# Performance work log

Measured on AMD Instinct MI355X. Metric: run time of the kernel, lower is better.

The kernel has to match this reference:

```python
import jax, jax.numpy as jnp
from jax import lax
import numpy as np

B, T, S = 64, 1024, 1024  # batch, seq_len, hidden size


def setup_inputs() -> dict:
    key = jax.random.key(0)
    ks = jax.random.split(key, 7)
    bound = 1.0 / np.sqrt(S)  # PyTorch GRU/Linear default init: U(-1/sqrt(H), 1/sqrt(H))
    u = lambda k, shape: jax.random.uniform(k, shape, jnp.float32, -bound, bound)
    return {
        "batch": jax.random.normal(ks[0], (B, T, S), jnp.float32),
        "W_ih": u(ks[1], (3 * S, S)),   # [r; z; n] input weights
        "W_hh": u(ks[2], (3 * S, S)),   # [r; z; n] hidden weights
        "b_ih": u(ks[3], (3 * S,)),
        "b_hh": u(ks[4], (3 * S,)),
        "W_out": u(ks[5], (1, S)),
        "b_out": u(ks[6], (1,)),
    }


def reference(batch, W_ih, W_hh, b_ih, b_hh, W_out, b_out):
    # Precompute input projections for all timesteps with one big GEMM: [B,T,3S]
    x_gates = jnp.einsum("bts,gs->btg", batch, W_ih) + b_ih

    def step(h, xg):
        # h: [B,S], xg: [B,3S]
        hg = h @ W_hh.T + b_hh                      # [B,3S]
        xr, xz, xn = jnp.split(xg, 3, axis=-1)
        hr, hz, hn = jnp.split(hg, 3, axis=-1)
        r = jax.nn.sigmoid(xr + hr)
        z = jax.nn.sigmoid(xz + hz)
        n = jnp.tanh(xn + r * hn)
        h_new = (1.0 - z) * n + z * h               # PyTorch GRU update
        return h_new, None

    h0 = jnp.zeros((batch.shape[0], S), batch.dtype)
    hT, _ = lax.scan(step, h0, jnp.swapaxes(x_gates, 0, 1))  # scan over time

    # last-timestep hidden -> linear -> sigmoid -> squeeze
    out = jax.nn.sigmoid(hT @ W_out.T + b_out)  # [B,1]
    return out.squeeze(-1)                      # [B]
```

## Files before the change

kernel.cpp:

```cpp
#include <hip/hip_runtime.h>
#include <math.h>


#define BB 64
#define TT 1024
#define SS 1024
#define GG (3 * SS)

__global__ void zero_kernel(float* __restrict__ p) {
  p[(size_t)blockIdx.x * 1024 + threadIdx.x] = 0.f;
}

__global__ __launch_bounds__(256) void xgates_kernel(
    const float* __restrict__ A, const float* __restrict__ W,
    const float* __restrict__ b_ih, const float* __restrict__ b_hh,
    float* __restrict__ C) {
  __shared__ float As[16][132];
  __shared__ float Bs[16][132];

  const int tid = threadIdx.x;
  const int n0 = blockIdx.x * 128;
  const int t0 = blockIdx.y * 2;
  const int tx = tid & 15;
  const int ty = tid >> 4;

  float acc[8][8];
#pragma unroll
  for (int i = 0; i < 8; ++i)
#pragma unroll
    for (int j = 0; j < 8; ++j) acc[i][j] = 0.f;

  for (int kt = 0; kt < SS / 16; ++kt) {
    const int k0 = kt * 16;
#pragma unroll
    for (int i = 0; i < 2; ++i) {
      const int idx = tid + i * 256;
      const int r = idx >> 2;
      const int kq = (idx & 3) * 4;
      float4 av = *(const float4*)&A[((size_t)(r & 63) * TT + t0 + (r >> 6)) * SS + k0 + kq];
      float4 bv = *(const float4*)&W[(size_t)(n0 + r) * SS + k0 + kq];
      As[kq + 0][r] = av.x; As[kq + 1][r] = av.y;
      As[kq + 2][r] = av.z; As[kq + 3][r] = av.w;
      Bs[kq + 0][r] = bv.x; Bs[kq + 1][r] = bv.y;
      Bs[kq + 2][r] = bv.z; Bs[kq + 3][r] = bv.w;
    }
    __syncthreads();
#pragma unroll
    for (int k = 0; k < 16; ++k) {
      float4 a0 = *(const float4*)&As[k][ty * 8];
      float4 a1 = *(const float4*)&As[k][ty * 8 + 4];
      float4 b0 = *(const float4*)&Bs[k][tx * 8];
      float4 b1 = *(const float4*)&Bs[k][tx * 8 + 4];
      float a[8] = {a0.x, a0.y, a0.z, a0.w, a1.x, a1.y, a1.z, a1.w};
      float b[8] = {b0.x, b0.y, b0.z, b0.w, b1.x, b1.y, b1.z, b1.w};
#pragma unroll
      for (int i = 0; i < 8; ++i)
#pragma unroll
        for (int j = 0; j < 8; ++j) acc[i][j] = fmaf(a[i], b[j], acc[i][j]);
    }
    __syncthreads();
  }

  float bias[8];
#pragma unroll
  for (int j = 0; j < 8; ++j) {
    const int n = n0 + tx * 8 + j;
    bias[j] = b_ih[n] + (n < 2 * SS ? b_hh[n] : 0.f);
  }
  const int tt = t0 + (ty >> 3);
  const int bbase = (ty & 7) * 8;
#pragma unroll
  for (int j = 0; j < 8; ++j) {
    const int n = n0 + tx * 8 + j;
    const int g = n >> 10;
    const int u = n & 1023;
    const size_t o = ((size_t)(tt * 3 + g) * SS + u) * 64 + bbase;
    *(float4*)&C[o] = make_float4(acc[0][j] + bias[j], acc[1][j] + bias[j],
                                  acc[2][j] + bias[j], acc[3][j] + bias[j]);
    *(float4*)&C[o + 4] = make_float4(acc[4][j] + bias[j], acc[5][j] + bias[j],
                                      acc[6][j] + bias[j], acc[7][j] + bias[j]);
  }
}

__global__ __launch_bounds__(1024) void gru_step_kernel(
    const float* __restrict__ hin, float* __restrict__ hout,
    const float* __restrict__ Whh, const float* __restrict__ xgT,
    const float* __restrict__ bhh, const int t) {
  __shared__ float part[16][64][13];
  __shared__ float sums[64][13];

  const int tid = threadIdx.x;
  const int lane = tid & 63;
  const int u0 = blockIdx.x * 4;
  const int wv = __builtin_amdgcn_readfirstlane(tid >> 6);
  const int k0 = wv * 64;

  const float* Wrow[12];
#pragma unroll
  for (int g = 0; g < 3; ++g)
#pragma unroll
    for (int r = 0; r < 4; ++r)
      Wrow[g * 4 + r] = Whh + (size_t)(g * SS + u0 + r) * SS + k0;

  float xr = 0.f, xz = 0.f, xn = 0.f, hold = 0.f, bhn = 0.f;
  if (tid < 256) {
    const int ur = tid >> 6;
    const size_t xb = ((size_t)(t * 3) * SS + u0 + ur) * 64 + (size_t)lane;
    xr = xgT[xb];
    xz = xgT[xb + (size_t)SS * 64];
    xn = xgT[xb + (size_t)2 * SS * 64];
    hold = hin[(u0 + ur) * 64 + lane];
    bhn = bhh[2 * SS + u0 + ur];
  }

  float acc[12];
#pragma unroll
  for (int i = 0; i < 12; ++i) acc[i] = 0.f;

  for (int kk = 0; kk < 64; kk += 8) {
    float hv[8];
#pragma unroll
    for (int e = 0; e < 8; ++e)
      hv[e] = hin[(size_t)(k0 + kk + e) * 64 + lane];
#pragma unroll
    for (int i = 0; i < 12; ++i) {
      const float* wp = Wrow[i] + kk;
      const float4 wa = *(const float4*)wp;
      const float4 wb = *(const float4*)(wp + 4);
      float a = acc[i];
      a = fmaf(hv[0], wa.x, a);
      a = fmaf(hv[1], wa.y, a);
      a = fmaf(hv[2], wa.z, a);
      a = fmaf(hv[3], wa.w, a);
      a = fmaf(hv[4], wb.x, a);
      a = fmaf(hv[5], wb.y, a);
      a = fmaf(hv[6], wb.z, a);
      a = fmaf(hv[7], wb.w, a);
      acc[i] = a;
    }
  }

  const int w = tid >> 6;
#pragma unroll
  for (int i = 0; i < 12; ++i) part[w][lane][i] = acc[i];
  __syncthreads();

  if (tid < 768) {
    const int sb = tid & 63, si = tid >> 6;
    float v = 0.f;
#pragma unroll
    for (int ww = 0; ww < 16; ++ww) v += part[ww][sb][si];
    sums[sb][si] = v;
  }
  __syncthreads();

  if (tid < 256) {
    const int ur = tid >> 6;
    const float ar = sums[lane][ur];
    const float az = sums[lane][4 + ur];
    const float an = sums[lane][8 + ur];
    const float rg = 1.f / (1.f + expf(-(xr + ar)));
    const float zg = 1.f / (1.f + expf(-(xz + az)));
    const float ng = tanhf(xn + rg * (an + bhn));
    hout[(u0 + ur) * 64 + lane] = (1.f - zg) * ng + zg * hold;
  }
}

__global__ __launch_bounds__(256) void out_kernel(
    const float* __restrict__ hT, const float* __restrict__ Wout,
    const float* __restrict__ bout, float* __restrict__ out) {
  const int b = blockIdx.x;
  const int tid = threadIdx.x;
  float s = 0.f;
#pragma unroll
  for (int i = 0; i < 4; ++i) {
    const int u = tid + i * 256;
    s = fmaf(hT[(size_t)u * 64 + b], Wout[u], s);
  }
#pragma unroll
  for (int off = 32; off; off >>= 1) s += __shfl_down(s, off);
  __shared__ float red[4];
  if ((tid & 63) == 0) red[tid >> 6] = s;
  __syncthreads();
  if (tid == 0) {
    const float tot = red[0] + red[1] + red[2] + red[3] + bout[0];
    out[b] = 1.f / (1.f + expf(-tot));
  }
}

extern "C" void kernel_launch(void* const* d_in, const int* in_sizes, int n_in,
                              void* d_out, int out_size, void* d_ws,
                              size_t ws_size, hipStream_t stream) {
  const float* batch = (const float*)d_in[0];
  const float* W_ih = (const float*)d_in[1];
  const float* W_hh = (const float*)d_in[2];
  const float* b_ih = (const float*)d_in[3];
  const float* b_hh = (const float*)d_in[4];
  const float* W_out = (const float*)d_in[5];
  const float* b_out = (const float*)d_in[6];
  float* out = (float*)d_out;

  float* xgT = (float*)d_ws;
  float* hA = xgT + (size_t)TT * GG * BB;
  float* hB = hA + (size_t)SS * BB;

  zero_kernel<<<BB, 1024, 0, stream>>>(hA);

  xgates_kernel<<<dim3(GG / 128, (BB * TT) / 128), 256, 0, stream>>>(
      batch, W_ih, b_ih, b_hh, xgT);

  for (int t = 0; t < TT; ++t) {
    const float* hp = (t & 1) ? hB : hA;
    float* hn = (t & 1) ? hA : hB;
    gru_step_kernel<<<256, 1024, 0, stream>>>(hp, hn, W_hh, xgT, b_hh, t);
  }

  out_kernel<<<BB, 256, 0, stream>>>(hA, W_out, b_out, out);
}
```

Measured before the change: 17.00 ms.

## Replace per-timestep GRU launches with one persistent cooperative kernel and grid barrier

Converts the 1024 separate GRU step launches into a single cooperative persistent kernel. Blocks loop over time and synchronise through a hierarchical atomic grid barrier (8 sub-counters feeding a generation flag). Hidden-state reads and writes become agent-scope atomics so they are visible across blocks. The next step's input gates are prefetched before the barrier. This removes launch overhead and the implicit sync between kernels, at the cost of a spin barrier whose correctness depends on all 256 blocks of 1024 threads being co-resident, and the barrier uses only a workgroup-scope acquire fence.

```diff
diff --git a/kernel.cpp b/kernel.cpp
--- a/kernel.cpp
+++ b/kernel.cpp
@@ -6,6 +6,17 @@
 #define TT 1024
 #define SS 1024
 #define GG (3 * SS)
+#define NBLK 256
+
+__device__ unsigned g_sub[8 * 32];
+__device__ unsigned g_cnt[32];
+__device__ unsigned g_gen[32];
+
+__global__ void init_bar_kernel() {
+  for (int i = 0; i < 8 * 32; ++i) g_sub[i] = 0u;
+  g_cnt[0] = 0u;
+  g_gen[0] = 0u;
+}
 
 __global__ void zero_kernel(float* __restrict__ p) {
   p[(size_t)blockIdx.x * 1024 + threadIdx.x] = 0.f;
@@ -82,10 +93,9 @@
   }
 }
 
-__global__ __launch_bounds__(1024) void gru_step_kernel(
-    const float* __restrict__ hin, float* __restrict__ hout,
+__global__ __launch_bounds__(1024) void gru_persistent(
     const float* __restrict__ Whh, const float* __restrict__ xgT,
-    const float* __restrict__ bhh, const int t) {
+    const float* __restrict__ bhh, float* hA, float* hB) {
   __shared__ float part[16][64][13];
   __shared__ float sums[64][13];
 
@@ -94,6 +104,7 @@
   const int u0 = blockIdx.x * 4;
   const int wv = __builtin_amdgcn_readfirstlane(tid >> 6);
   const int k0 = wv * 64;
+  const int ur = tid >> 6;
 
   const float* Wrow[12];
 #pragma unroll
@@ -102,67 +113,108 @@
     for (int r = 0; r < 4; ++r)
       Wrow[g * 4 + r] = Whh + (size_t)(g * SS + u0 + r) * SS + k0;
 
-  float xr = 0.f, xz = 0.f, xn = 0.f, hold = 0.f, bhn = 0.f;
+  float bhn = 0.f, xr = 0.f, xz = 0.f, xn = 0.f;
   if (tid < 256) {
-    const int ur = tid >> 6;
-    const size_t xb = ((size_t)(t * 3) * SS + u0 + ur) * 64 + (size_t)lane;
+    bhn = bhh[2 * SS + u0 + ur];
+    const size_t xb = (size_t)(u0 + ur) * 64 + (size_t)lane;
     xr = xgT[xb];
     xz = xgT[xb + (size_t)SS * 64];
     xn = xgT[xb + (size_t)2 * SS * 64];
-    hold = hin[(u0 + ur) * 64 + lane];
-    bhn = bhh[2 * SS + u0 + ur];
-  }
-
-  float acc[12];
-#pragma unroll
-  for (int i = 0; i < 12; ++i) acc[i] = 0.f;
-
-  for (int kk = 0; kk < 64; kk += 8) {
-    float hv[8];
-#pragma unroll
-    for (int e = 0; e < 8; ++e)
-      hv[e] = hin[(size_t)(k0 + kk + e) * 64 + lane];
-#pragma unroll
-    for (int i = 0; i < 12; ++i) {
-      const float* wp = Wrow[i] + kk;
-      const float4 wa = *(const float4*)wp;
-      const float4 wb = *(const float4*)(wp + 4);
-      float a = acc[i];
-      a = fmaf(hv[0], wa.x, a);
-      a = fmaf(hv[1], wa.y, a);
-      a = fmaf(hv[2], wa.z, a);
-      a = fmaf(hv[3], wa.w, a);
-      a = fmaf(hv[4], wb.x, a);
-      a = fmaf(hv[5], wb.y, a);
-      a = fmaf(hv[6], wb.z, a);
-      a = fmaf(hv[7], wb.w, a);
-      acc[i] = a;
-    }
-  }
-
-  const int w = tid >> 6;
-#pragma unroll
-  for (int i = 0; i < 12; ++i) part[w][lane][i] = acc[i];
-  __syncthreads();
-
-  if (tid < 768) {
-    const int sb = tid & 63, si = tid >> 6;
-    float v = 0.f;
-#pragma unroll
-    for (int ww = 0; ww < 16; ++ww) v += part[ww][sb][si];
-    sums[sb][si] = v;
-  }
-  __syncthreads();
-
-  if (tid < 256) {
-    const int ur = tid >> 6;
-    const float ar = sums[lane][ur];
-    const float az = sums[lane][4 + ur];
-    const float an = sums[lane][8 + ur];
-    const float rg = 1.f / (1.f + expf(-(xr + ar)));
-    const float zg = 1.f / (1.f + expf(-(xz + az)));
-    const float ng = tanhf(xn + rg * (an + bhn));
-    hout[(u0 + ur) * 64 + lane] = (1.f - zg) * ng + zg * hold;
+  }
+
+  for (int t = 0; t < TT; ++t) {
+    float* hin = (t & 1) ? hB : hA;
+    float* hout = (t & 1) ? hA : hB;
+
+    float hold = 0.f;
+    if (tid < 256)
+      hold = __hip_atomic_load(&hin[(u0 + ur) * 64 + lane], __ATOMIC_RELAXED,
+                               __HIP_MEMORY_SCOPE_AGENT);
+
+    float acc[12];
+#pragma unroll
+    for (int i = 0; i < 12; ++i) acc[i] = 0.f;
+
+    for (int kk = 0; kk < 64; kk += 8) {
+      float hv[8];
+#pragma unroll
+      for (int e = 0; e < 8; ++e)
+        hv[e] = __hip_atomic_load(&hin[(size_t)(k0 + kk + e) * 64 + lane],
+                                  __ATOMIC_RELAXED, __HIP_MEMORY_SCOPE_AGENT);
+#pragma unroll
+      for (int i = 0; i < 12; ++i) {
+        const float* wp = Wrow[i] + kk;
+        const float4 wa = *(const float4*)wp;
+        const float4 wb = *(const float4*)(wp + 4);
+        float a = acc[i];
+        a = fmaf(hv[0], wa.x, a);
+        a = fmaf(hv[1], wa.y, a);
+        a = fmaf(hv[2], wa.z, a);
+        a = fmaf(hv[3], wa.w, a);
+        a = fmaf(hv[4], wb.x, a);
+        a = fmaf(hv[5], wb.y, a);
+        a = fmaf(hv[6], wb.z, a);
+        a = fmaf(hv[7], wb.w, a);
+        acc[i] = a;
+      }
+    }
+
+    const int w = tid >> 6;
+#pragma unroll
+    for (int i = 0; i < 12; ++i) part[w][lane][i] = acc[i];
+    __syncthreads();
+
+    if (tid < 768) {
+      const int sb = tid & 63, si = tid >> 6;
+      float v = 0.f;
+#pragma unroll
+      for (int ww = 0; ww < 16; ++ww) v += part[ww][sb][si];
+      sums[sb][si] = v;
+    }
+    __syncthreads();
+
+    if (tid < 256) {
+      const float ar = sums[lane][ur];
+      const float az = sums[lane][4 + ur];
+      const float an = sums[lane][8 + ur];
+      const float rg = 1.f / (1.f + expf(-(xr + ar)));
+      const float zg = 1.f / (1.f + expf(-(xz + az)));
+      const float ng = tanhf(xn + rg * (an + bhn));
+      const float hnew = (1.f - zg) * ng + zg * hold;
+      __hip_atomic_store(&hout[(u0 + ur) * 64 + lane], hnew, __ATOMIC_RELAXED,
+                         __HIP_MEMORY_SCOPE_AGENT);
+      if (t + 1 < TT) {
+        const size_t xb =
+            ((size_t)((t + 1) * 3) * SS + u0 + ur) * 64 + (size_t)lane;
+        xr = xgT[xb];
+        xz = xgT[xb + (size_t)SS * 64];
+        xn = xgT[xb + (size_t)2 * SS * 64];
+      }
+    }
+
+    if (t != TT - 1) {
+      __syncthreads();
+      if (tid == 0) {
+        bool done = false;
+        const unsigned a = atomicAdd(&g_sub[(blockIdx.x & 7) * 32], 1u);
+        if (a == 32u * (unsigned)(t + 1) - 1u) {
+          const unsigned g = atomicAdd(&g_cnt[0], 1u);
+          if (g == 8u * (unsigned)(t + 1) - 1u) {
+            __hip_atomic_store(&g_gen[0], (unsigned)(t + 1), __ATOMIC_RELAXED,
+                               __HIP_MEMORY_SCOPE_AGENT);
+            done = true;
+          }
+        }
+        if (!done) {
+          while (__hip_atomic_load(&g_gen[0], __ATOMIC_RELAXED,
+                                   __HIP_MEMORY_SCOPE_AGENT) <
+                 (unsigned)(t + 1))
+            __builtin_amdgcn_s_sleep(2);
+        }
+        __builtin_amdgcn_fence(__ATOMIC_ACQUIRE, "workgroup");
+      }
+      __syncthreads();
+    }
   }
 }
 
@@ -204,15 +256,21 @@
   float* hA = xgT + (size_t)TT * GG * BB;
   float* hB = hA + (size_t)SS * BB;
 
+  init_bar_kernel<<<1, 1, 0, stream>>>();
   zero_kernel<<<BB, 1024, 0, stream>>>(hA);
 
   xgates_kernel<<<dim3(GG / 128, (BB * TT) / 128), 256, 0, stream>>>(
       batch, W_ih, b_ih, b_hh, xgT);
 
-  for (int t = 0; t < TT; ++t) {
-    const float* hp = (t & 1) ? hB : hA;
-    float* hn = (t & 1) ? hA : hB;
-    gru_step_kernel<<<256, 1024, 0, stream>>>(hp, hn, W_hh, xgT, b_hh, t);
+  {
+    const float* a0 = W_hh;
+    const float* a1 = xgT;
+    const float* a2 = b_hh;
+    float* a3 = hA;
+    float* a4 = hB;
+    void* args[5] = {&a0, &a1, &a2, &a3, &a4};
+    hipLaunchCooperativeKernel((const void*)gru_persistent, dim3(NBLK),
+                               dim3(1024), args, 0, stream);
   }
 
   out_kernel<<<BB, 256, 0, stream>>>(hA, W_out, b_out, out);
```

New measurement: 17.20 ms. About the same (+1.2%).
